# Kernel tuning notes

Measured on AMD Instinct MI355X. Metric: run time of the kernel, lower is better.

The kernel has to match this reference:

```python
import jax, jax.numpy as jnp
import numpy as np

N = 200000          # total nodes
G = 512             # num graphs (segments)
D = 256             # in_dim == h_dim == sum_dim
OUT = 128           # head out_dim
L = 4               # depth
EPS = 1e-5


def setup_inputs() -> dict:
    key = jax.random.key(0)
    ks = jax.random.split(key, 12)
    x = jax.random.normal(ks[0], (N, D), dtype=jnp.float32)
    batch = jnp.sort(jax.random.randint(ks[1], (N,), 0, G)).astype(jnp.int32)
    s = 0.06  # ~xavier scale for 256-wide layers
    return {
        "x": x,
        "batch": batch,
        "phi_w1": s * jax.random.normal(ks[2], (L, D, D), dtype=jnp.float32),
        "phi_b1": jnp.zeros((L, D), jnp.float32),
        "phi_ln_g": jnp.ones((L, D), jnp.float32),
        "phi_ln_b": jnp.zeros((L, D), jnp.float32),
        "phi_w2": s * jax.random.normal(ks[3], (L, D, D), dtype=jnp.float32),
        "phi_b2": jnp.zeros((L, D), jnp.float32),
        "psi_w1": s * jax.random.normal(ks[4], (L, 2 * D, D), dtype=jnp.float32),
        "psi_b1": jnp.zeros((L, D), jnp.float32),
        "psi_ln_g": jnp.ones((L, D), jnp.float32),
        "psi_ln_b": jnp.zeros((L, D), jnp.float32),
        "psi_w2": s * jax.random.normal(ks[5], (L, D, D), dtype=jnp.float32),
        "psi_b2": jnp.zeros((L, D), jnp.float32),
        "out_ln_g": jnp.ones((L, D), jnp.float32),
        "out_ln_b": jnp.zeros((L, D), jnp.float32),
        "head_w": s * jax.random.normal(ks[6], (D, OUT), dtype=jnp.float32),
        "head_b": jnp.zeros((OUT,), jnp.float32),
    }


def _ln(h, g, b):
    mu = jnp.mean(h, axis=-1, keepdims=True)
    var = jnp.mean(jnp.square(h - mu), axis=-1, keepdims=True)
    return (h - mu) * jax.lax.rsqrt(var + EPS) * g + b


def _mlp(h, w1, b1, g, beta, w2, b2):
    # Linear -> ReLU -> LayerNorm -> Linear (MLP with num_layers=2, use_ln=True)
    h = jax.nn.relu(h @ w1 + b1)
    h = _ln(h, g, beta)
    return h @ w2 + b2


def reference(x, batch, phi_w1, phi_b1, phi_ln_g, phi_ln_b, phi_w2, phi_b2,
              psi_w1, psi_b1, psi_ln_g, psi_ln_b, psi_w2, psi_b2,
              out_ln_g, out_ln_b, head_w, head_b):
    for i in range(L):
        phi_x = _mlp(x, phi_w1[i], phi_b1[i], phi_ln_g[i], phi_ln_b[i], phi_w2[i], phi_b2[i])
        # global_add_pool: scatter-add per graph, then gather back to nodes
        gsum = jax.ops.segment_sum(phi_x, batch, num_segments=G)   # [G, D]
        expanded = gsum[batch]                                      # [N, D]
        combined = jnp.concatenate([x, expanded], axis=-1)          # [N, 2D]
        out = _mlp(combined, psi_w1[i], psi_b1[i], psi_ln_g[i], psi_ln_b[i], psi_w2[i], psi_b2[i])
        out = x + out                                               # residual (in_dim == out_dim)
        x = _ln(out, out_ln_g[i], out_ln_b[i])                      # out_ln
    return x @ head_w + head_b
```

## Files before the change

kernel.cpp:

```cpp
#include <hip/hip_runtime.h>
#include <stdint.h>

#define DEV __device__ __forceinline__

constexpr int NN = 200000;
constexpr int GSEG = 512;

typedef __attribute__((ext_vector_type(8)))  short   s8v;
typedef __attribute__((ext_vector_type(4)))  float   f4v;
typedef __attribute__((ext_vector_type(16))) float   f16v;
typedef __attribute__((ext_vector_type(4)))  unsigned short u4v;
typedef __attribute__((ext_vector_type(4)))  _Float16 h4v;

DEV void mfma32(const s8v& a, const s8v& b, f16v& c){
  asm volatile("v_mfma_f32_32x32x16_bf16 %0, %1, %2, %0" : "+v"(c) : "v"(a), "v"(b));
}

DEV unsigned short f2bs(float f){
  union { float f; uint32_t u; } v; v.f = f;
  uint32_t u = v.u;
  u = u + 0x7fffu + ((u >> 16) & 1u);
  return (unsigned short)(u >> 16);
}
DEV float b2f(unsigned short s){
  union { uint32_t u; float f; } v; v.u = ((uint32_t)s) << 16;
  return v.f;
}
DEV unsigned short f2h(float f){
  union{ _Float16 h; unsigned short u; } v; v.h = (_Float16)f; return v.u;
}
DEV s8v cvt8(f4v a, f4v b){
  s8v r;
  r[0]=(short)f2bs(a[0]); r[1]=(short)f2bs(a[1]); r[2]=(short)f2bs(a[2]); r[3]=(short)f2bs(a[3]);
  r[4]=(short)f2bs(b[0]); r[5]=(short)f2bs(b[1]); r[6]=(short)f2bs(b[2]); r[7]=(short)f2bs(b[3]);
  return r;
}

DEV void gload_lds16(const void* g, void* l){
  __builtin_amdgcn_global_load_lds(
      (const __attribute__((address_space(1))) void*)g,
      (__attribute__((address_space(3))) void*)l, 16, 0, 0);
}

DEV u4v shfl_xor32_u4(u4v v){
  union { u4v q; long long l; } a, b;
  a.q = v;
  b.l = __shfl_xor(a.l, 32);
  return b.q;
}


template<int BSRC>
DEV s8v load_bfrag(const unsigned short* Xb, const float* Xf, const float* gsum,
                   int row, int g, int k16, int h){
  if constexpr(BSRC==0){
    return *(const s8v*)(Xb + (size_t)(row>>5)*8192 + (size_t)(k16*2+h)*256 + (row&31)*8);
  } else if constexpr(BSRC==1){
    const float* p = Xf + (size_t)row*256 + k16*16 + h*8;
    return cvt8(*(const f4v*)p, *(const f4v*)(p+4));
  } else if constexpr(BSRC==2){
    if(k16 < 16)
      return *(const s8v*)(Xb + (size_t)(row>>5)*8192 + (size_t)(k16*2+h)*256 + (row&31)*8);
    const float* p = gsum + (size_t)g*256 + (k16-16)*16 + h*8;
    return cvt8(*(const f4v*)p, *(const f4v*)(p+4));
  } else {
    if(k16 < 16){
      const float* p = Xf + (size_t)row*256 + k16*16 + h*8;
      return cvt8(*(const f4v*)p, *(const f4v*)(p+4));
    }
    const float* p = gsum + (size_t)g*256 + (k16-16)*16 + h*8;
    return cvt8(*(const f4v*)p, *(const f4v*)(p+4));
  }
}

template<int DOUT,int KDIM,int BSRC,int MODE,int RES,int WRH>
__global__ __launch_bounds__(256,2) void gemm_ln(
    const unsigned short* Xb, const float* Xf, const float* gsumIn, const int* batch,
    const unsigned short* PW, const float* bias, const float* lng, const float* lnb,
    const float* xresf, const unsigned short* xresh, const unsigned short* xresb,
    unsigned short* outb, unsigned short* outh, float* outf)
{
  constexpr int NM  = DOUT/32;
  constexpr int NI  = DOUT/64;
  constexpr int CHB = NM*4096;
  constexpr int ITER= CHB/4096;
  __shared__ __align__(16) char smem[CHB + 2048];
  __shared__ __align__(16) char sT[(MODE==2) ? 32768 : 16];

  const int tid  = threadIdx.x;
  const int lane = tid & 63;
  const int wid  = tid >> 6;
  const int wr = wid >> 1, wc = wid & 1;
  const int l32 = lane & 31, h = lane >> 5;
  const int rb   = (int)blockIdx.x * 128;
  const int row0 = rb + wr*64 + l32;
  const int row1 = row0 + 32;
  const int r0c = row0 < NN ? row0 : NN-1;
  const int r1c = row1 < NN ? row1 : NN-1;

  f16v acc[2][NI];
  #pragma unroll
  for(int ni=0; ni<NI; ++ni){
    #pragma unroll
    for(int rq=0; rq<4; ++rq){
      f4v bv = *(const f4v*)(bias + wc*(DOUT/2) + ni*32 + 8*rq + 4*h);
      #pragma unroll
      for(int j=0;j<4;++j){ acc[0][ni][rq*4+j]=bv[j]; acc[1][ni][rq*4+j]=bv[j]; }
    }
  }

  int g0=0, g1=0;
  if constexpr(BSRC>=2){ g0 = batch[r0c]; g1 = batch[r1c]; }

  for(int kc=0; kc<KDIM/64; ++kc){
    const unsigned short* src = PW + (size_t)kc*(CHB/2);
    #pragma unroll
    for(int it=0; it<ITER; ++it){
      int idx = it*256 + tid;
      gload_lds16(src + (size_t)idx*8, smem + (it*256 + wid*64)*16);
    }
    __syncthreads();
    #pragma unroll
    for(int k2=0;k2<4;++k2){
      const int k16 = kc*4 + k2;
      s8v b0 = load_bfrag<BSRC>(Xb, Xf, gsumIn, r0c, g0, k16, h);
      s8v b1 = load_bfrag<BSRC>(Xb, Xf, gsumIn, r1c, g1, k16, h);
      #pragma unroll
      for(int ni=0; ni<NI; ++ni){
        s8v a = *(const s8v*)(smem + ((k2*NM + wc*NI + ni)*64 + lane)*16);
        mfma32(a, b0, acc[0][ni]);
        mfma32(a, b1, acc[1][ni]);
      }
    }
    __syncthreads();
  }

  if constexpr(MODE==0 || MODE==1){
    #pragma unroll
    for(int nj=0;nj<2;++nj){
      if constexpr(MODE==1){
        const int rr = nj ? r1c : r0c;
        #pragma unroll
        for(int ni=0;ni<NI;++ni){
          #pragma unroll
          for(int rq=0;rq<4;++rq){
            const int c4 = wc*(DOUT/2) + ni*32 + 8*rq + 4*h;
            f4v rv;
            if constexpr(RES==1){
              rv = *(const f4v*)(xresf + (size_t)rr*256 + c4);
            } else if constexpr(RES==2){
              const int o = wc*16 + ni*4 + rq;
              h4v hv = *(const h4v*)(xresh + (size_t)(rr>>5)*8192 + (size_t)o*256 + (rr&31)*8 + 4*h);
              #pragma unroll
              for(int j=0;j<4;++j) rv[j] = (float)hv[j];
            } else {
              const int o = wc*16 + ni*4 + rq;
              u4v u = *(const u4v*)(xresb + (size_t)(rr>>5)*8192 + (size_t)o*256 + (rr&31)*8 + 4*h);
              #pragma unroll
              for(int j=0;j<4;++j) rv[j] = b2f(u[j]);
            }
            #pragma unroll
            for(int j=0;j<4;++j) acc[nj][ni][rq*4+j] += rv[j];
          }
        }
      } else {
        #pragma unroll
        for(int ni=0;ni<NI;++ni)
          #pragma unroll
          for(int r=0;r<16;++r) acc[nj][ni][r] = fmaxf(acc[nj][ni][r], 0.f);
      }
    }
    float s[2]={0.f,0.f}, q[2]={0.f,0.f};
    #pragma unroll
    for(int nj=0;nj<2;++nj)
      #pragma unroll
      for(int ni=0;ni<NI;++ni)
        #pragma unroll
        for(int r=0;r<16;++r){ float v = acc[nj][ni][r]; s[nj]+=v; q[nj]=fmaf(v,v,q[nj]); }
    #pragma unroll
    for(int nj=0;nj<2;++nj){ s[nj] += __shfl_xor(s[nj],32); q[nj] += __shfl_xor(q[nj],32); }
    float2* st = (float2*)(smem + CHB);
    if(lane < 32){
      st[(((wr*2+0)*32)+lane)*2 + wc] = make_float2(s[0], q[0]);
      st[(((wr*2+1)*32)+lane)*2 + wc] = make_float2(s[1], q[1]);
    }
    __syncthreads();
    float mu[2], rs[2];
    #pragma unroll
    for(int nj=0;nj<2;++nj){
      f4v v = *(const f4v*)(st + (((wr*2+nj)*32)+l32)*2);
      float S = v[0]+v[2], Q = v[1]+v[3];
      mu[nj] = S*(1.f/256.f);
      float var = Q*(1.f/256.f) - mu[nj]*mu[nj];
      rs[nj] = rsqrtf(var + 1e-5f);
    }
    #pragma unroll
    for(int nj=0;nj<2;++nj){
      const int rowS = nj ? row1 : row0;
      #pragma unroll
      for(int t=0;t<8;++t){
        const int niE = (16*t)>>5,     rqE = (2*t)&3;
        const int niO = (16*t+8)>>5,   rqO = (2*t+1)&3;
        f4v fe, fo;
        {
          const int c4 = wc*(DOUT/2) + niE*32 + 8*rqE + 4*h;
          f4v gv = *(const f4v*)(lng + c4);
          f4v bv = *(const f4v*)(lnb + c4);
          #pragma unroll
          for(int j=0;j<4;++j)
            fe[j] = fmaf((acc[nj][niE][rqE*4+j]-mu[nj])*rs[nj], gv[j], bv[j]);
        }
        {
          const int c4 = wc*(DOUT/2) + niO*32 + 8*rqO + 4*h;
          f4v gv = *(const f4v*)(lng + c4);
          f4v bv = *(const f4v*)(lnb + c4);
          #pragma unroll
          for(int j=0;j<4;++j)
            fo[j] = fmaf((acc[nj][niO][rqO*4+j]-mu[nj])*rs[nj], gv[j], bv[j]);
        }
        const int o = wc*16 + 2*t + h;
        unsigned short* dst = outb + (size_t)(rowS>>5)*8192 + (size_t)o*256 + (rowS&31)*8;
        {
          u4v qe, qo;
          #pragma unroll
          for(int j=0;j<4;++j){ qe[j] = f2bs(fe[j]); qo[j] = f2bs(fo[j]); }
          u4v snd = h ? qe : qo;
          u4v rcv = shfl_xor32_u4(snd);
          u4v lo4 = h ? rcv : qe;
          u4v hi4 = h ? qo  : rcv;
          if(rowS < NN){
            s8v ov;
            #pragma unroll
            for(int j=0;j<4;++j){ ov[j] = (short)lo4[j]; ov[4+j] = (short)hi4[j]; }
            *(s8v*)dst = ov;
          }
        }
        if constexpr(WRH){
          u4v qe, qo;
          #pragma unroll
          for(int j=0;j<4;++j){ qe[j] = f2h(fe[j]); qo[j] = f2h(fo[j]); }
          u4v snd = h ? qe : qo;
          u4v rcv = shfl_xor32_u4(snd);
          u4v lo4 = h ? rcv : qe;
          u4v hi4 = h ? qo  : rcv;
          if(rowS < NN){
            s8v ov;
            #pragma unroll
            for(int j=0;j<4;++j){ ov[j] = (short)lo4[j]; ov[4+j] = (short)hi4[j]; }
            *(s8v*)(outh + (size_t)(rowS>>5)*8192 + (size_t)o*256 + (rowS&31)*8) = ov;
          }
        }
      }
    }
  } else {
    for(int chunk=0; chunk<2; ++chunk){
      if(chunk) __syncthreads();
      if(wr == chunk){
        #pragma unroll
        for(int nj=0;nj<2;++nj){
          #pragma unroll
          for(int ni=0;ni<NI;++ni){
            #pragma unroll
            for(int rq=0;rq<4;++rq){
              const int c4 = wc*(DOUT/2) + ni*32 + 8*rq + 4*h;
              f4v o;
              #pragma unroll
              for(int j=0;j<4;++j) o[j] = acc[nj][ni][rq*4+j];
              *(f4v*)(sT + (nj*32+l32)*512 + ((c4*4) ^ (l32<<4))) = o;
            }
          }
        }
      }
      __syncthreads();
      #pragma unroll
      for(int i=0;i<8;++i){
        const int r = i*8 + (tid>>5);
        const int c = tid & 31;
        const int grow = rb + chunk*64 + r;
        if(grow < NN)
          *(f4v*)(outf + (size_t)grow*DOUT + c*4) =
              *(const f4v*)(sT + r*512 + ((c*16) ^ ((r&31)<<4)));
      }
    }
  }
}

__global__ __launch_bounds__(256,2) void gemm_segsum(
    const unsigned short* Xb, const unsigned short* PW, const float* bias,
    const int* batch, float* gsum)
{
  __shared__ __align__(16) char smem[32768];
  const int tid = threadIdx.x, lane = tid&63, wid = tid>>6;
  const int wr = wid>>1, wc = wid&1, l32 = lane&31, h = lane>>5;
  const int rb = (int)blockIdx.x*128;
  const int ra0 = rb + wr*64 + l32;
  const int ra1 = ra0 + 32;
  const int r0c = ra0 < NN ? ra0 : NN-1;
  const int r1c = ra1 < NN ? ra1 : NN-1;
  const int browi = rb + wr*64 + lane;
  const int b_l = (browi < NN) ? batch[browi] : 0x7fffffff;

  f16v acc[2][4];
  #pragma unroll
  for(int n=0;n<4;++n){
    float bv = bias[wc*128 + n*32 + l32];
    #pragma unroll
    for(int m=0;m<2;++m)
      #pragma unroll
      for(int r=0;r<16;++r) acc[m][n][r] = bv;
  }

  for(int kc=0; kc<4; ++kc){
    const unsigned short* src = PW + (size_t)kc*16384;
    #pragma unroll
    for(int it=0; it<8; ++it){
      int idx = it*256 + tid;
      gload_lds16(src + (size_t)idx*8, smem + (it*256 + wid*64)*16);
    }
    __syncthreads();
    #pragma unroll
    for(int k2=0;k2<4;++k2){
      const int k16 = kc*4+k2;
      s8v a0 = *(const s8v*)(Xb + (size_t)(r0c>>5)*8192 + (size_t)(k16*2+h)*256 + (r0c&31)*8);
      s8v a1 = *(const s8v*)(Xb + (size_t)(r1c>>5)*8192 + (size_t)(k16*2+h)*256 + (r1c&31)*8);
      #pragma unroll
      for(int n=0;n<4;++n){
        s8v bw = *(const s8v*)(smem + ((k2*8 + wc*4 + n)*64 + lane)*16);
        mfma32(a0, bw, acc[0][n]);
        mfma32(a1, bw, acc[1][n]);
      }
    }
    __syncthreads();
  }

  int lo = 0;
  while(lo < 64){
    int g = __shfl(b_l, lo);
    unsigned long long mb = __ballot(b_l == g);
    int hi = lo + __popcll(mb);
    if(g < GSEG){
      #pragma unroll
      for(int n=0;n<4;++n){
        float sum = 0.f;
        #pragma unroll
        for(int m=0;m<2;++m){
          if(hi <= m*32 || lo >= m*32+32) continue;
          #pragma unroll
          for(int r=0;r<16;++r){
            int lr = m*32 + (r&3) + 8*(r>>2) + 4*h;
            sum += (lr >= lo && lr < hi) ? acc[m][n][r] : 0.f;
          }
        }
        sum += __shfl_xor(sum, 32);
        if(lane < 32) atomicAdd(&gsum[(size_t)g*256 + wc*128 + n*32 + lane], sum);
      }
    }
    lo = hi;
  }
}

__global__ void pack_weights(const float* phi_w1, const float* phi_w2,
                             const float* psi_w1, const float* psi_w2,
                             const float* head_w, unsigned short* pw)
{
  int o = (int)blockIdx.x*256 + (int)threadIdx.x;
  if(o >= 167936) return;
  const float* src; unsigned short* dst; int Dout, oo;
  if(o < 32768){        int l=o>>13;            oo=o&8191;  src=phi_w1+(size_t)l*65536;  dst=pw+(size_t)l*65536;           Dout=256; }
  else if(o < 65536){   int t=o-32768,l=t>>13;  oo=t&8191;  src=phi_w2+(size_t)l*65536;  dst=pw+262144+(size_t)l*65536;    Dout=256; }
  else if(o < 131072){  int t=o-65536,l=t>>14;  oo=t&16383; src=psi_w1+(size_t)l*131072; dst=pw+524288+(size_t)l*131072;   Dout=256; }
  else if(o < 163840){  int t=o-131072,l=t>>13; oo=t&8191;  src=psi_w2+(size_t)l*65536;  dst=pw+1048576+(size_t)l*65536;   Dout=256; }
  else{                 oo=o-163840;            src=head_w; dst=pw+1310720;                                                Dout=128; }
  const int NM = Dout/32;
  int lane = oo & 63;
  int m   = (oo>>6) % NM;
  int k16 = (oo>>6) / NM;
  int kb  = k16*16 + (lane>>5)*8;
  int col = m*32 + (lane&31);
  #pragma unroll
  for(int jj=0;jj<8;++jj) dst[(size_t)oo*8 + jj] = f2bs(src[(size_t)(kb+jj)*Dout + col]);
}

extern "C" void kernel_launch(void* const* d_in, const int* in_sizes, int n_in,
                              void* d_out, int out_size, void* d_ws, size_t ws_size,
                              hipStream_t stream)
{
  (void)in_sizes; (void)n_in; (void)out_size;
  const float* x0       = (const float*)d_in[0];
  const int*   batch    = (const int*)  d_in[1];
  const float* phi_w1   = (const float*)d_in[2];
  const float* phi_b1   = (const float*)d_in[3];
  const float* phi_ln_g = (const float*)d_in[4];
  const float* phi_ln_b = (const float*)d_in[5];
  const float* phi_w2   = (const float*)d_in[6];
  const float* phi_b2   = (const float*)d_in[7];
  const float* psi_w1   = (const float*)d_in[8];
  const float* psi_b1   = (const float*)d_in[9];
  const float* psi_ln_g = (const float*)d_in[10];
  const float* psi_ln_b = (const float*)d_in[11];
  const float* psi_w2   = (const float*)d_in[12];
  const float* psi_b2   = (const float*)d_in[13];
  const float* out_ln_g = (const float*)d_in[14];
  const float* out_ln_b = (const float*)d_in[15];
  const float* head_w   = (const float*)d_in[16];
  const float* head_b   = (const float*)d_in[17];

  char* ws = (char*)d_ws;
  unsigned short* pw = (unsigned short*)ws;
  float* gsum        = (float*)(ws + 4194304);
  unsigned short* hb = (unsigned short*)(ws + 8388608);
  const bool dual = (ws_size >= 315588608ull);
  unsigned short* xb = dual ? (unsigned short*)(ws + 110788608)
                            : (unsigned short*)d_out;
  unsigned short* xh = dual ? (unsigned short*)(ws + 213188608) : nullptr;

  const int grid = (NN + 127)/128;

  pack_weights<<<656,256,0,stream>>>(phi_w1, phi_w2, psi_w1, psi_w2, head_w, pw);

  for(int l=0;l<4;++l){
    const unsigned short* pw_phi1 = pw + (size_t)l*65536;
    const unsigned short* pw_phi2 = pw + 262144 + (size_t)l*65536;
    const unsigned short* pw_psi1 = pw + 524288 + (size_t)l*131072;
    const unsigned short* pw_psi2 = pw + 1048576 + (size_t)l*65536;
    const float* b1 = phi_b1 + l*256, *g1 = phi_ln_g + l*256, *n1 = phi_ln_b + l*256;
    const float* b2 = phi_b2 + l*256;
    const float* p1 = psi_b1 + l*256, *pg = psi_ln_g + l*256, *pn = psi_ln_b + l*256;
    const float* p2 = psi_b2 + l*256;
    const float* og = out_ln_g + l*256, *on = out_ln_b + l*256;

    if(l==0)
      gemm_ln<256,256,1,0,0,0><<<grid,256,0,stream>>>(nullptr, x0, nullptr, nullptr,
          pw_phi1, b1, g1, n1, nullptr, nullptr, nullptr, hb, nullptr, nullptr);
    else
      gemm_ln<256,256,0,0,0,0><<<grid,256,0,stream>>>(xb, nullptr, nullptr, nullptr,
          pw_phi1, b1, g1, n1, nullptr, nullptr, nullptr, hb, nullptr, nullptr);

    hipMemsetAsync(gsum, 0, 524288, stream);
    gemm_segsum<<<grid,256,0,stream>>>(hb, pw_phi2, b2, batch, gsum);

    if(l==0)
      gemm_ln<256,512,3,0,0,0><<<grid,256,0,stream>>>(nullptr, x0, gsum, batch,
          pw_psi1, p1, pg, pn, nullptr, nullptr, nullptr, hb, nullptr, nullptr);
    else
      gemm_ln<256,512,2,0,0,0><<<grid,256,0,stream>>>(xb, nullptr, gsum, batch,
          pw_psi1, p1, pg, pn, nullptr, nullptr, nullptr, hb, nullptr, nullptr);

    if(l==0){
      if(dual)
        gemm_ln<256,256,0,1,1,1><<<grid,256,0,stream>>>(hb, nullptr, nullptr, nullptr,
            pw_psi2, p2, og, on, x0, nullptr, nullptr, xb, xh, nullptr);
      else
        gemm_ln<256,256,0,1,1,0><<<grid,256,0,stream>>>(hb, nullptr, nullptr, nullptr,
            pw_psi2, p2, og, on, x0, nullptr, nullptr, xb, nullptr, nullptr);
    } else if(l<3){
      if(dual)
        gemm_ln<256,256,0,1,2,1><<<grid,256,0,stream>>>(hb, nullptr, nullptr, nullptr,
            pw_psi2, p2, og, on, nullptr, xh, nullptr, xb, xh, nullptr);
      else
        gemm_ln<256,256,0,1,3,0><<<grid,256,0,stream>>>(hb, nullptr, nullptr, nullptr,
            pw_psi2, p2, og, on, nullptr, nullptr, xb, xb, nullptr, nullptr);
    } else {
      if(dual)
        gemm_ln<256,256,0,1,2,0><<<grid,256,0,stream>>>(hb, nullptr, nullptr, nullptr,
            pw_psi2, p2, og, on, nullptr, xh, nullptr, xb, nullptr, nullptr);
      else
        gemm_ln<256,256,0,1,3,0><<<grid,256,0,stream>>>(hb, nullptr, nullptr, nullptr,
            pw_psi2, p2, og, on, nullptr, nullptr, xb, xb, nullptr, nullptr);
    }
  }

  gemm_ln<128,256,0,2,0,0><<<grid,256,0,stream>>>(xb, nullptr, nullptr, nullptr,
      pw + 1310720, head_b, nullptr, nullptr, nullptr, nullptr, nullptr,
      nullptr, nullptr, (float*)d_out);
}
```

Before: 1.516 ms.

## Use persistent LDS-resident-weight GEMM kernels and precompute per-graph psi contribution

Replaces the per-tile GEMM+LN kernels with persistent 512-thread blocks that load the whole 256x256 bf16 weight matrix into 128KB of LDS once and loop over 256-row tiles. This removes the repeated per-chunk weight staging and its barriers. It also splits the psi first layer algebraically: the gsum half of the matmul is computed once per graph (512 rows) in a small gy kernel, and each node's accumulator is initialised from gy[batch]. That halves the K dimension of the largest GEMM. The costs are one block per CU, limited latency hiding, and an extra small launch.

After: 1.410 ms (median of 2 runs). -7.0%, faster.

```diff
diff --git a/kernel.cpp b/kernel.cpp
--- a/kernel.cpp
+++ b/kernel.cpp
@@ -5,6 +5,8 @@
 
 constexpr int NN = 200000;
 constexpr int GSEG = 512;
+constexpr int PTILES = (NN + 255) / 256;
+constexpr int GRID_P = 256;
 
 typedef __attribute__((ext_vector_type(8)))  short   s8v;
 typedef __attribute__((ext_vector_type(4)))  float   f4v;
@@ -73,78 +75,77 @@
   }
 }
 
-template<int DOUT,int KDIM,int BSRC,int MODE,int RES,int WRH>
-__global__ __launch_bounds__(256,2) void gemm_ln(
-    const unsigned short* Xb, const float* Xf, const float* gsumIn, const int* batch,
+template<int BSRC,int MODE,int RES,int WRH,int INITG>
+__global__ __launch_bounds__(512,1) void gemm_pers(
+    const unsigned short* Xb, const float* Xf, const float* gyIn, const int* batch,
     const unsigned short* PW, const float* bias, const float* lng, const float* lnb,
     const float* xresf, const unsigned short* xresh, const unsigned short* xresb,
-    unsigned short* outb, unsigned short* outh, float* outf)
+    unsigned short* outb, unsigned short* outh, int ntiles)
 {
-  constexpr int NM  = DOUT/32;
-  constexpr int NI  = DOUT/64;
-  constexpr int CHB = NM*4096;
-  constexpr int ITER= CHB/4096;
-  __shared__ __align__(16) char smem[CHB + 2048];
-  __shared__ __align__(16) char sT[(MODE==2) ? 32768 : 16];
-
-  const int tid  = threadIdx.x;
-  const int lane = tid & 63;
-  const int wid  = tid >> 6;
+  __shared__ __align__(16) char sW[131072];
+  __shared__ __align__(16) float2 sStat[2][8][32][2];
+
+  const int tid = threadIdx.x, lane = tid & 63, wid = tid >> 6;
   const int wr = wid >> 1, wc = wid & 1;
   const int l32 = lane & 31, h = lane >> 5;
-  const int rb   = (int)blockIdx.x * 128;
-  const int row0 = rb + wr*64 + l32;
-  const int row1 = row0 + 32;
-  const int r0c = row0 < NN ? row0 : NN-1;
-  const int r1c = row1 < NN ? row1 : NN-1;
-
-  f16v acc[2][NI];
+
   #pragma unroll
-  for(int ni=0; ni<NI; ++ni){
-    #pragma unroll
-    for(int rq=0; rq<4; ++rq){
-      f4v bv = *(const f4v*)(bias + wc*(DOUT/2) + ni*32 + 8*rq + 4*h);
-      #pragma unroll
-      for(int j=0;j<4;++j){ acc[0][ni][rq*4+j]=bv[j]; acc[1][ni][rq*4+j]=bv[j]; }
-    }
-  }
-
-  int g0=0, g1=0;
-  if constexpr(BSRC>=2){ g0 = batch[r0c]; g1 = batch[r1c]; }
-
-  for(int kc=0; kc<KDIM/64; ++kc){
-    const unsigned short* src = PW + (size_t)kc*(CHB/2);
-    #pragma unroll
-    for(int it=0; it<ITER; ++it){
-      int idx = it*256 + tid;
-      gload_lds16(src + (size_t)idx*8, smem + (it*256 + wid*64)*16);
-    }
-    __syncthreads();
-    #pragma unroll
-    for(int k2=0;k2<4;++k2){
-      const int k16 = kc*4 + k2;
-      s8v b0 = load_bfrag<BSRC>(Xb, Xf, gsumIn, r0c, g0, k16, h);
-      s8v b1 = load_bfrag<BSRC>(Xb, Xf, gsumIn, r1c, g1, k16, h);
-      #pragma unroll
-      for(int ni=0; ni<NI; ++ni){
-        s8v a = *(const s8v*)(smem + ((k2*NM + wc*NI + ni)*64 + lane)*16);
+  for(int it=0; it<16; ++it)
+    gload_lds16(PW + (size_t)(it*512 + wid*64 + lane)*8,
+                sW + (it*512 + wid*64)*16);
+  __syncthreads();
+
+  int tp = 0;
+  for(int t = (int)blockIdx.x; t < ntiles; t += (int)gridDim.x, tp ^= 1){
+    const int rb   = t * 256;
+    const int row0 = rb + wr*64 + l32;
+    const int row1 = row0 + 32;
+    const int r0c = row0 < NN ? row0 : NN-1;
+    const int r1c = row1 < NN ? row1 : NN-1;
+
+    int g0=0, g1=0;
+    if constexpr(INITG){ g0 = batch[r0c]; g1 = batch[r1c]; }
+
+    f16v acc[2][4];
+    #pragma unroll
+    for(int ni=0; ni<4; ++ni){
+      #pragma unroll
+      for(int rq=0; rq<4; ++rq){
+        const int c4 = wc*128 + ni*32 + 8*rq + 4*h;
+        if constexpr(INITG){
+          f4v a0 = *(const f4v*)(gyIn + (size_t)g0*256 + c4);
+          f4v a1 = *(const f4v*)(gyIn + (size_t)g1*256 + c4);
+          #pragma unroll
+          for(int j=0;j<4;++j){ acc[0][ni][rq*4+j]=a0[j]; acc[1][ni][rq*4+j]=a1[j]; }
+        } else {
+          f4v bv = *(const f4v*)(bias + c4);
+          #pragma unroll
+          for(int j=0;j<4;++j){ acc[0][ni][rq*4+j]=bv[j]; acc[1][ni][rq*4+j]=bv[j]; }
+        }
+      }
+    }
+
+    #pragma unroll 4
+    for(int k16=0; k16<16; ++k16){
+      s8v b0 = load_bfrag<BSRC>(Xb, Xf, nullptr, r0c, 0, k16, h);
+      s8v b1 = load_bfrag<BSRC>(Xb, Xf, nullptr, r1c, 0, k16, h);
+      #pragma unroll
+      for(int ni=0; ni<4; ++ni){
+        s8v a = *(const s8v*)(sW + ((k16*8 + wc*4 + ni)*64 + lane)*16);
         mfma32(a, b0, acc[0][ni]);
         mfma32(a, b1, acc[1][ni]);
       }
     }
-    __syncthreads();
-  }
-
-  if constexpr(MODE==0 || MODE==1){
+
     #pragma unroll
     for(int nj=0;nj<2;++nj){
       if constexpr(MODE==1){
         const int rr = nj ? r1c : r0c;
         #pragma unroll
-        for(int ni=0;ni<NI;++ni){
+        for(int ni=0;ni<4;++ni){
           #pragma unroll
           for(int rq=0;rq<4;++rq){
-            const int c4 = wc*(DOUT/2) + ni*32 + 8*rq + 4*h;
+            const int c4 = wc*128 + ni*32 + 8*rq + 4*h;
             f4v rv;
             if constexpr(RES==1){
               rv = *(const f4v*)(xresf + (size_t)rr*256 + c4);
@@ -165,7 +166,7 @@
         }
       } else {
         #pragma unroll
-        for(int ni=0;ni<NI;++ni)
+        for(int ni=0;ni<4;++ni)
           #pragma unroll
           for(int r=0;r<16;++r) acc[nj][ni][r] = fmaxf(acc[nj][ni][r], 0.f);
       }
@@ -174,21 +175,20 @@
     #pragma unroll
     for(int nj=0;nj<2;++nj)
       #pragma unroll
-      for(int ni=0;ni<NI;++ni)
+      for(int ni=0;ni<4;++ni)
         #pragma unroll
         for(int r=0;r<16;++r){ float v = acc[nj][ni][r]; s[nj]+=v; q[nj]=fmaf(v,v,q[nj]); }
     #pragma unroll
     for(int nj=0;nj<2;++nj){ s[nj] += __shfl_xor(s[nj],32); q[nj] += __shfl_xor(q[nj],32); }
-    float2* st = (float2*)(smem + CHB);
     if(lane < 32){
-      st[(((wr*2+0)*32)+lane)*2 + wc] = make_float2(s[0], q[0]);
-      st[(((wr*2+1)*32)+lane)*2 + wc] = make_float2(s[1], q[1]);
+      sStat[tp][wr*2+0][lane][wc] = make_float2(s[0], q[0]);
+      sStat[tp][wr*2+1][lane][wc] = make_float2(s[1], q[1]);
     }
     __syncthreads();
     float mu[2], rs[2];
     #pragma unroll
     for(int nj=0;nj<2;++nj){
-      f4v v = *(const f4v*)(st + (((wr*2+nj)*32)+l32)*2);
+      f4v v = *(const f4v*)(&sStat[tp][wr*2+nj][l32][0]);
       float S = v[0]+v[2], Q = v[1]+v[3];
       mu[nj] = S*(1.f/256.f);
       float var = Q*(1.f/256.f) - mu[nj]*mu[nj];
@@ -198,12 +198,12 @@
     for(int nj=0;nj<2;++nj){
       const int rowS = nj ? row1 : row0;
       #pragma unroll
-      for(int t=0;t<8;++t){
-        const int niE = (16*t)>>5,     rqE = (2*t)&3;
-        const int niO = (16*t+8)>>5,   rqO = (2*t+1)&3;
+      for(int ot=0;ot<8;++ot){
+        const int niE = (16*ot)>>5,     rqE = (2*ot)&3;
+        const int niO = (16*ot+8)>>5,   rqO = (2*ot+1)&3;
         f4v fe, fo;
         {
-          const int c4 = wc*(DOUT/2) + niE*32 + 8*rqE + 4*h;
+          const int c4 = wc*128 + niE*32 + 8*rqE + 4*h;
           f4v gv = *(const f4v*)(lng + c4);
           f4v bv = *(const f4v*)(lnb + c4);
           #pragma unroll
@@ -211,15 +211,14 @@
             fe[j] = fmaf((acc[nj][niE][rqE*4+j]-mu[nj])*rs[nj], gv[j], bv[j]);
         }
         {
-          const int c4 = wc*(DOUT/2) + niO*32 + 8*rqO + 4*h;
+          const int c4 = wc*128 + niO*32 + 8*rqO + 4*h;
           f4v gv = *(const f4v*)(lng + c4);
           f4v bv = *(const f4v*)(lnb + c4);
           #pragma unroll
           for(int j=0;j<4;++j)
             fo[j] = fmaf((acc[nj][niO][rqO*4+j]-mu[nj])*rs[nj], gv[j], bv[j]);
         }
-        const int o = wc*16 + 2*t + h;
-        unsigned short* dst = outb + (size_t)(rowS>>5)*8192 + (size_t)o*256 + (rowS&31)*8;
+        const int o = wc*16 + 2*ot + h;
         {
           u4v qe, qo;
           #pragma unroll
@@ -232,7 +231,7 @@
             s8v ov;
             #pragma unroll
             for(int j=0;j<4;++j){ ov[j] = (short)lo4[j]; ov[4+j] = (short)hi4[j]; }
-            *(s8v*)dst = ov;
+            *(s8v*)(outb + (size_t)(rowS>>5)*8192 + (size_t)o*256 + (rowS&31)*8) = ov;
           }
         }
         if constexpr(WRH){
@@ -252,66 +251,106 @@
         }
       }
     }
-  } else {
-    for(int chunk=0; chunk<2; ++chunk){
-      if(chunk) __syncthreads();
-      if(wr == chunk){
+  }
+}
+
+__global__ __launch_bounds__(512,1) void segsum_pers(
+    const unsigned short* Xb, const unsigned short* PW, const float* bias,
+    const int* batch, float* gsum, int ntiles)
+{
+  __shared__ __align__(16) char sW[131072];
+  const int tid = threadIdx.x, lane = tid & 63, wid = tid >> 6;
+  const int wr = wid >> 1, wc = wid & 1;
+  const int l32 = lane & 31, h = lane >> 5;
+
+  #pragma unroll
+  for(int it=0; it<16; ++it)
+    gload_lds16(PW + (size_t)(it*512 + wid*64 + lane)*8,
+                sW + (it*512 + wid*64)*16);
+  __syncthreads();
+
+  for(int t = (int)blockIdx.x; t < ntiles; t += (int)gridDim.x){
+    const int rb = t * 256;
+    const int ra0 = rb + wr*64 + l32;
+    const int ra1 = ra0 + 32;
+    const int r0c = ra0 < NN ? ra0 : NN-1;
+    const int r1c = ra1 < NN ? ra1 : NN-1;
+    const int browi = rb + wr*64 + lane;
+    const int b_l = (browi < NN) ? batch[browi] : 0x7fffffff;
+
+    f16v acc[2][4];
+    #pragma unroll
+    for(int n=0;n<4;++n){
+      float bv = bias[wc*128 + n*32 + l32];
+      #pragma unroll
+      for(int m=0;m<2;++m)
         #pragma unroll
-        for(int nj=0;nj<2;++nj){
-          #pragma unroll
-          for(int ni=0;ni<NI;++ni){
+        for(int r=0;r<16;++r) acc[m][n][r] = bv;
+    }
+
+    #pragma unroll 4
+    for(int k16=0; k16<16; ++k16){
+      s8v a0 = *(const s8v*)(Xb + (size_t)(r0c>>5)*8192 + (size_t)(k16*2+h)*256 + (r0c&31)*8);
+      s8v a1 = *(const s8v*)(Xb + (size_t)(r1c>>5)*8192 + (size_t)(k16*2+h)*256 + (r1c&31)*8);
+      #pragma unroll
+      for(int n=0;n<4;++n){
+        s8v bw = *(const s8v*)(sW + ((k16*8 + wc*4 + n)*64 + lane)*16);
+        mfma32(a0, bw, acc[0][n]);
+        mfma32(a1, bw, acc[1][n]);
+      }
+    }
+
+    int lo = 0;
+    while(lo < 64){
+      int g = __shfl(b_l, lo);
+      unsigned long long mb = __ballot(b_l == g);
+      int hi = lo + __popcll(mb);
+      if(g < GSEG){
+        #pragma unroll
+        for(int n=0;n<4;++n){
+          float sum = 0.f;
+          #pragma unroll
+          for(int m=0;m<2;++m){
+            if(hi <= m*32 || lo >= m*32+32) continue;
             #pragma unroll
-            for(int rq=0;rq<4;++rq){
-              const int c4 = wc*(DOUT/2) + ni*32 + 8*rq + 4*h;
-              f4v o;
-              #pragma unroll
-              for(int j=0;j<4;++j) o[j] = acc[nj][ni][rq*4+j];
-              *(f4v*)(sT + (nj*32+l32)*512 + ((c4*4) ^ (l32<<4))) = o;
+            for(int r=0;r<16;++r){
+              int lr = m*32 + (r&3) + 8*(r>>2) + 4*h;
+              sum += (lr >= lo && lr < hi) ? acc[m][n][r] : 0.f;
             }
           }
-        }
-      }
-      __syncthreads();
-      #pragma unroll
-      for(int i=0;i<8;++i){
-        const int r = i*8 + (tid>>5);
-        const int c = tid & 31;
-        const int grow = rb + chunk*64 + r;
-        if(grow < NN)
-          *(f4v*)(outf + (size_t)grow*DOUT + c*4) =
-              *(const f4v*)(sT + r*512 + ((c*16) ^ ((r&31)<<4)));
-      }
-    }
-  }
-}
-
-__global__ __launch_bounds__(256,2) void gemm_segsum(
-    const unsigned short* Xb, const unsigned short* PW, const float* bias,
-    const int* batch, float* gsum)
+          sum += __shfl_xor(sum, 32);
+          if(lane < 32) atomicAdd(&gsum[(size_t)g*256 + wc*128 + n*32 + lane], sum);
+        }
+      }
+      lo = hi;
+    }
+  }
+}
+
+__global__ __launch_bounds__(256,2) void gy_k(
+    const float* gsum, const unsigned short* PWhi, const float* bias, float* gy)
 {
   __shared__ __align__(16) char smem[32768];
-  const int tid = threadIdx.x, lane = tid&63, wid = tid>>6;
-  const int wr = wid>>1, wc = wid&1, l32 = lane&31, h = lane>>5;
-  const int rb = (int)blockIdx.x*128;
-  const int ra0 = rb + wr*64 + l32;
-  const int ra1 = ra0 + 32;
-  const int r0c = ra0 < NN ? ra0 : NN-1;
-  const int r1c = ra1 < NN ? ra1 : NN-1;
-  const int browi = rb + wr*64 + lane;
-  const int b_l = (browi < NN) ? batch[browi] : 0x7fffffff;
+  const int tid = threadIdx.x, lane = tid & 63, wid = tid >> 6;
+  const int wr = wid >> 1, wc = wid & 1;
+  const int l32 = lane & 31, h = lane >> 5;
+  const int rb = (int)blockIdx.x * 128;
+  const int row0 = rb + wr*64 + l32;
+  const int row1 = row0 + 32;
 
   f16v acc[2][4];
   #pragma unroll
-  for(int n=0;n<4;++n){
-    float bv = bias[wc*128 + n*32 + l32];
-    #pragma unroll
-    for(int m=0;m<2;++m)
-      #pragma unroll
-      for(int r=0;r<16;++r) acc[m][n][r] = bv;
+  for(int ni=0;ni<4;++ni){
+    #pragma unroll
+    for(int rq=0;rq<4;++rq){
+      f4v bv = *(const f4v*)(bias + wc*128 + ni*32 + 8*rq + 4*h);
+      #pragma unroll
+      for(int j=0;j<4;++j){ acc[0][ni][rq*4+j]=bv[j]; acc[1][ni][rq*4+j]=bv[j]; }
+    }
   }
 
   for(int kc=0; kc<4; ++kc){
-    const unsigned short* src = PW + (size_t)kc*16384;
+    const unsigned short* src = PWhi + (size_t)kc*16384;
     #pragma unroll
     for(int it=0; it<8; ++it){
       int idx = it*256 + tid;
@@ -320,42 +359,128 @@
     __syncthreads();
     #pragma unroll
     for(int k2=0;k2<4;++k2){
-      const int k16 = kc*4+k2;
-      s8v a0 = *(const s8v*)(Xb + (size_t)(r0c>>5)*8192 + (size_t)(k16*2+h)*256 + (r0c&31)*8);
-      s8v a1 = *(const s8v*)(Xb + (size_t)(r1c>>5)*8192 + (size_t)(k16*2+h)*256 + (r1c&31)*8);
-      #pragma unroll
-      for(int n=0;n<4;++n){
-        s8v bw = *(const s8v*)(smem + ((k2*8 + wc*4 + n)*64 + lane)*16);
-        mfma32(a0, bw, acc[0][n]);
-        mfma32(a1, bw, acc[1][n]);
+      const int k16 = kc*4 + k2;
+      const float* p0 = gsum + (size_t)row0*256 + k16*16 + h*8;
+      const float* p1 = gsum + (size_t)row1*256 + k16*16 + h*8;
+      s8v b0 = cvt8(*(const f4v*)p0, *(const f4v*)(p0+4));
+      s8v b1 = cvt8(*(const f4v*)p1, *(const f4v*)(p1+4));
+      #pragma unroll
+      for(int ni=0;ni<4;++ni){
+        s8v a = *(const s8v*)(smem + ((k2*8 + wc*4 + ni)*64 + lane)*16);
+        mfma32(a, b0, acc[0][ni]);
+        mfma32(a, b1, acc[1][ni]);
       }
     }
     __syncthreads();
   }
 
-  int lo = 0;
-  while(lo < 64){
-    int g = __shfl(b_l, lo);
-    unsigned long long mb = __ballot(b_l == g);
-    int hi = lo + __popcll(mb);
-    if(g < GSEG){
-      #pragma unroll
-      for(int n=0;n<4;++n){
-        float sum = 0.f;
+  #pragma unroll
+  for(int nj=0;nj<2;++nj){
+    const int rowS = nj ? row1 : row0;
+    #pragma unroll
+    for(int ni=0;ni<4;++ni){
+      #pragma unroll
+      for(int rq=0;rq<4;++rq){
+        const int c4 = wc*128 + ni*32 + 8*rq + 4*h;
+        f4v o;
         #pragma unroll
-        for(int m=0;m<2;++m){
-          if(hi <= m*32 || lo >= m*32+32) continue;
-          #pragma unroll
-          for(int r=0;r<16;++r){
-            int lr = m*32 + (r&3) + 8*(r>>2) + 4*h;
-            sum += (lr >= lo && lr < hi) ? acc[m][n][r] : 0.f;
+        for(int j=0;j<4;++j) o[j] = acc[nj][ni][rq*4+j];
+        *(f4v*)(gy + (size_t)rowS*256 + c4) = o;
+      }
+    }
+  }
+}
+
+template<int DOUT,int KDIM,int BSRC,int MODE,int RES,int WRH>
+__global__ __launch_bounds__(256,2) void gemm_ln(
+    const unsigned short* Xb, const float* Xf, const float* gsumIn, const int* batch,
+    const unsigned short* PW, const float* bias, const float* lng, const float* lnb,
+    const float* xresf, const unsigned short* xresh, const unsigned short* xresb,
+    unsigned short* outb, unsigned short* outh, float* outf)
+{
+  constexpr int NM  = DOUT/32;
+  constexpr int NI  = DOUT/64;
+  constexpr int CHB = NM*4096;
+  constexpr int ITER= CHB/4096;
+  __shared__ __align__(16) char smem[CHB + 2048];
+  __shared__ __align__(16) char sT[(MODE==2) ? 32768 : 16];
+
+  const int tid  = threadIdx.x;
+  const int lane = tid & 63;
+  const int wid  = tid >> 6;
+  const int wr = wid >> 1, wc = wid & 1;
+  const int l32 = lane & 31, h = lane >> 5;
+  const int rb   = (int)blockIdx.x * 128;
+  const int row0 = rb + wr*64 + l32;
+  const int row1 = row0 + 32;
+  const int r0c = row0 < NN ? row0 : NN-1;
+  const int r1c = row1 < NN ? row1 : NN-1;
+
+  f16v acc[2][NI];
+  #pragma unroll
+  for(int ni=0; ni<NI; ++ni){
+    #pragma unroll
+    for(int rq=0; rq<4; ++rq){
+      f4v bv = *(const f4v*)(bias + wc*(DOUT/2) + ni*32 + 8*rq + 4*h);
+      #pragma unroll
+      for(int j=0;j<4;++j){ acc[0][ni][rq*4+j]=bv[j]; acc[1][ni][rq*4+j]=bv[j]; }
+    }
+  }
+
+  int g0=0, g1=0;
+  if constexpr(BSRC>=2){ g0 = batch[r0c]; g1 = batch[r1c]; }
+
+  for(int kc=0; kc<KDIM/64; ++kc){
+    const unsigned short* src = PW + (size_t)kc*(CHB/2);
+    #pragma unroll
+    for(int it=0; it<ITER; ++it){
+      int idx = it*256 + tid;
+      gload_lds16(src + (size_t)idx*8, smem + (it*256 + wid*64)*16);
+    }
+    __syncthreads();
+    #pragma unroll
+    for(int k2=0;k2<4;++k2){
+      const int k16 = kc*4 + k2;
+      s8v b0 = load_bfrag<BSRC>(Xb, Xf, gsumIn, r0c, g0, k16, h);
+      s8v b1 = load_bfrag<BSRC>(Xb, Xf, gsumIn, r1c, g1, k16, h);
+      #pragma unroll
+      for(int ni=0; ni<NI; ++ni){
+        s8v a = *(const s8v*)(smem + ((k2*NM + wc*NI + ni)*64 + lane)*16);
+        mfma32(a, b0, acc[0][ni]);
+        mfma32(a, b1, acc[1][ni]);
+      }
+    }
+    __syncthreads();
+  }
+
+  for(int chunk=0; chunk<2; ++chunk){
+    if(chunk) __syncthreads();
+    if(wr == chunk){
+      #pragma unroll
+      for(int nj=0;nj<2;++nj){
+        #pragma unroll
+        for(int ni=0;ni<NI;++ni){
+          #pragma unroll
+          for(int rq=0;rq<4;++rq){
+            const int c4 = wc*(DOUT/2) + ni*32 + 8*rq + 4*h;
+            f4v o;
+            #pragma unroll
+            for(int j=0;j<4;++j) o[j] = acc[nj][ni][rq*4+j];
+            *(f4v*)(sT + (nj*32+l32)*512 + ((c4*4) ^ (l32<<4))) = o;
           }
         }
-        sum += __shfl_xor(sum, 32);
-        if(lane < 32) atomicAdd(&gsum[(size_t)g*256 + wc*128 + n*32 + lane], sum);
-      }
-    }
-    lo = hi;
+      }
+    }
+    __syncthreads();
+    #pragma unroll
+    for(int i=0;i<8;++i){
+      const int r = i*8 + (tid>>5);
+      const int c = tid & 31;
+      const int grow = rb + chunk*64 + r;
+      if(grow < NN)
+        *(f4v*)(outf + (size_t)grow*DOUT + c*4) =
+            *(const f4v*)(sT + r*512 + ((c*16) ^ ((r&31)<<4)));
+    }
   }
 }
 
@@ -408,13 +533,12 @@
   char* ws = (char*)d_ws;
   unsigned short* pw = (unsigned short*)ws;
   float* gsum        = (float*)(ws + 4194304);
+  float* gy          = (float*)(ws + 4718592);
   unsigned short* hb = (unsigned short*)(ws + 8388608);
   const bool dual = (ws_size >= 315588608ull);
   unsigned short* xb = dual ? (unsigned short*)(ws + 110788608)
                             : (unsigned short*)d_out;
   unsigned short* xh = dual ? (unsigned short*)(ws + 213188608) : nullptr;
-
-  const int grid = (NN + 127)/128;
 
   pack_weights<<<656,256,0,stream>>>(phi_w1, phi_w2, psi_w1, psi_w2, head_w, pw);
 
@@ -430,47 +554,49 @@
     const float* og = out_ln_g + l*256, *on = out_ln_b + l*256;
 
     if(l==0)
-      gemm_ln<256,256,1,0,0,0><<<grid,256,0,stream>>>(nullptr, x0, nullptr, nullptr,
-          pw_phi1, b1, g1, n1, nullptr, nullptr, nullptr, hb, nullptr, nullptr);
+      gemm_pers<1,0,0,0,0><<<GRID_P,512,0,stream>>>(nullptr, x0, nullptr, nullptr,
+          pw_phi1, b1, g1, n1, nullptr, nullptr, nullptr, hb, nullptr, PTILES);
     else
-      gemm_ln<256,256,0,0,0,0><<<grid,256,0,stream>>>(xb, nullptr, nullptr, nullptr,
-          pw_phi1, b1, g1, n1, nullptr, nullptr, nullptr, hb, nullptr, nullptr);
+      gemm_pers<0,0,0,0,0><<<GRID_P,512,0,stream>>>(xb, nullptr, nullptr, nullptr,
+          pw_phi1, b1, g1, n1, nullptr, nullptr, nullptr, hb, nullptr, PTILES);
 
     hipMemsetAsync(gsum, 0, 524288, stream);
-    gemm_segsum<<<grid,256,0,stream>>>(hb, pw_phi2, b2, batch, gsum);
+    segsum_pers<<<GRID_P,512,0,stream>>>(hb, pw_phi2, b2, batch, gsum, PTILES);
+
+    gy_k<<<4,256,0,stream>>>(gsum, pw_psi1 + 65536, p1, gy);
 
     if(l==0)
-      gemm_ln<256,512,3,0,0,0><<<grid,256,0,stream>>>(nullptr, x0, gsum, batch,
-          pw_psi1, p1, pg, pn, nullptr, nullptr, nullptr, hb, nullptr, nullptr);
+      gemm_pers<1,0,0,0,1><<<GRID_P,512,0,stream>>>(nullptr, x0, gy, batch,
+          pw_psi1, nullptr, pg, pn, nullptr, nullptr, nullptr, hb, nullptr, PTILES);
     else
-      gemm_ln<256,512,2,0,0,0><<<grid,256,0,stream>>>(xb, nullptr, gsum, batch,
-          pw_psi1, p1, pg, pn, nullptr, nullptr, nullptr, hb, nullptr, nullptr);
+      gemm_pers<0,0,0,0,1><<<GRID_P,512,0,stream>>>(xb, nullptr, gy, batch,
+          pw_psi1, nullptr, pg, pn, nullptr, nullptr, nullptr, hb, nullptr, PTILES);
 
     if(l==0){
       if(dual)
-        gemm_ln<256,256,0,1,1,1><<<grid,256,0,stream>>>(hb, nullptr, nullptr, nullptr,
-            pw_psi2, p2, og, on, x0, nullptr, nullptr, xb, xh, nullptr);
+        gemm_pers<0,1,1,1,0><<<GRID_P,512,0,stream>>>(hb, nullptr, nullptr, nullptr,
+            pw_psi2, p2, og, on, x0, nullptr, nullptr, xb, xh, PTILES);
       else
-        gemm_ln<256,256,0,1,1,0><<<grid,256,0,stream>>>(hb, nullptr, nullptr, nullptr,
-            pw_psi2, p2, og, on, x0, nullptr, nullptr, xb, nullptr, nullptr);
+        gemm_pers<0,1,1,0,0><<<GRID_P,512,0,stream>>>(hb, nullptr, nullptr, nullptr,
+            pw_psi2, p2, og, on, x0, nullptr, nullptr, xb, nullptr, PTILES);
     } else if(l<3){
       if(dual)
-        gemm_ln<256,256,0,1,2,1><<<grid,256,0,stream>>>(hb, nullptr, nullptr, nullptr,
-            pw_psi2, p2, og, on, nullptr, xh, nullptr, xb, xh, nullptr);
+        gemm_pers<0,1,2,1,0><<<GRID_P,512,0,stream>>>(hb, nullptr, nullptr, nullptr,
+            pw_psi2, p2, og, on, nullptr, xh, nullptr, xb, xh, PTILES);
       else
-        gemm_ln<256,256,0,1,3,0><<<grid,256,0,stream>>>(hb, nullptr, nullptr, nullptr,
-            pw_psi2, p2, og, on, nullptr, nullptr, xb, xb, nullptr, nullptr);
+        gemm_pers<0,1,3,0,0><<<GRID_P,512,0,stream>>>(hb, nullptr, nullptr, nullptr,
+            pw_psi2, p2, og, on, nullptr, nullptr, xb, xb, nullptr, PTILES);
     } else {
       if(dual)
-        gemm_ln<256,256,0,1,2,0><<<grid,256,0,stream>>>(hb, nullptr, nullptr, nullptr,
-            pw_psi2, p2, og, on, nullptr, xh, nullptr, xb, nullptr, nullptr);
+        gemm_pers<0,1,2,0,0><<<GRID_P,512,0,stream>>>(hb, nullptr, nullptr, nullptr,
+            pw_psi2, p2, og, on, nullptr, xh, nullptr, xb, nullptr, PTILES);
       else
-        gemm_ln<256,256,0,1,3,0><<<grid,256,0,stream>>>(hb, nullptr, nullptr, nullptr,
-            pw_psi2, p2, og, on, nullptr, nullptr, xb, xb, nullptr, nullptr);
-    }
-  }
-
-  gemm_ln<128,256,0,2,0,0><<<grid,256,0,stream>>>(xb, nullptr, nullptr, nullptr,
+        gemm_pers<0,1,3,0,0><<<GRID_P,512,0,stream>>>(hb, nullptr, nullptr, nullptr,
+            pw_psi2, p2, og, on, nullptr, nullptr, xb, xb, nullptr, PTILES);
+    }
+  }
+
+  gemm_ln<128,256,0,2,0,0><<<(NN+127)/128,256,0,stream>>>(xb, nullptr, nullptr, nullptr,
       pw + 1310720, head_b, nullptr, nullptr, nullptr, nullptr, nullptr,
       nullptr, nullptr, (float*)d_out);
 }
```
